# Kernel tuning notes

Hardware: AMD Instinct MI355X
Metric: run time of the kernel (lower is better)

The kernel has to match this reference:

```python
import jax, jax.numpy as jnp
import numpy as np
import math

B = 2        # batch
S = 4095     # input sequence (cls token makes L = 4096)
F_IN = 32    # input feature size
D = 512      # d_model (hidden_size)
H = 8        # n_heads
E = D // H   # head dim = 64
DFF = 2048   # feedforward dim
NL = 2       # encoder layers
FACTOR = 5   # probsparse sampling factor
EPS = 1e-5


def setup_inputs() -> dict:
    key = jax.random.key(0)
    ks = jax.random.split(key, 16)

    def w(k, shape):
        return jax.random.normal(k, shape, dtype=jnp.float32) * 0.02

    inp = {}
    inp['x'] = jax.random.normal(ks[0], (B, S, F_IN), dtype=jnp.float32)
    inp['We'] = w(ks[1], (D, F_IN)); inp['be'] = jnp.zeros((D,), jnp.float32)
    inp['cls'] = jnp.zeros((1, 1, D), jnp.float32)
    inp['Wq'] = w(ks[2], (NL, D, D)); inp['bq'] = jnp.zeros((NL, D), jnp.float32)
    inp['Wk'] = w(ks[3], (NL, D, D)); inp['bk'] = jnp.zeros((NL, D), jnp.float32)
    inp['Wv'] = w(ks[4], (NL, D, D)); inp['bv'] = jnp.zeros((NL, D), jnp.float32)
    inp['Wo'] = w(ks[5], (NL, D, D)); inp['bo'] = jnp.zeros((NL, D), jnp.float32)
    inp['g1'] = jnp.ones((NL, D), jnp.float32); inp['b1'] = jnp.zeros((NL, D), jnp.float32)
    inp['g2'] = jnp.ones((NL, D), jnp.float32); inp['b2'] = jnp.zeros((NL, D), jnp.float32)
    inp['W1'] = w(ks[6], (NL, DFF, D)); inp['bf1'] = jnp.zeros((NL, DFF), jnp.float32)
    inp['W2'] = w(ks[7], (NL, D, DFF)); inp['bf2'] = jnp.zeros((NL, D), jnp.float32)
    inp['Wf'] = w(ks[8], (1, D)); inp['bf'] = jnp.zeros((1,), jnp.float32)
    return inp


def pos_encoding(L):
    # Sinusoidal positional encoding [L, D]
    pos = jnp.arange(L, dtype=jnp.float32)[:, None]
    div = jnp.exp(jnp.arange(0, D, 2, dtype=jnp.float32) * (-math.log(10000.0) / D))
    pe = jnp.zeros((L, D), jnp.float32)
    pe = pe.at[:, 0::2].set(jnp.sin(pos * div))
    pe = pe.at[:, 1::2].set(jnp.cos(pos * div))
    return pe


def layer_norm(x, g, b):
    mu = x.mean(-1, keepdims=True)
    var = ((x - mu) ** 2).mean(-1, keepdims=True)
    return (x - mu) / jnp.sqrt(var + EPS) * g + b


def prob_attention(q, k, v, rng):
    # q, k, v: [B, H, L, E]; mask_flag=False (encoder self-attention)
    b, h, L, e = q.shape
    u = min(FACTOR * int(np.ceil(np.log(L))), L)  # sample_k == n_top here (L_Q == L_K)
    idx = jax.random.randint(rng, (L, u), 0, L)   # random K sampling per query position
    Ks = k[:, :, idx, :]                          # [B,H,L,u,E] gather
    QKs = jnp.einsum('bhle,bhlue->bhlu', q, Ks)   # sampled scores
    M = QKs.max(-1) - QKs.sum(-1) / L             # sparsity measure [B,H,L]
    _, top = jax.lax.top_k(M, u)                  # active query indices [B,H,u]
    Qr = jnp.take_along_axis(q, top[..., None], axis=2)      # [B,H,u,E]
    scores = jnp.einsum('bhue,bhke->bhuk', Qr, k) / math.sqrt(e)
    attn = jax.nn.softmax(scores, axis=-1)
    ctx = jnp.broadcast_to(v.mean(axis=2, keepdims=True), (b, h, L, e))  # initial context = mean(V)
    upd = jnp.einsum('bhuk,bhke->bhue', attn, v)
    bi = jnp.arange(b)[:, None, None]
    hi = jnp.arange(h)[None, :, None]
    ctx = ctx.at[bi, hi, top].set(upd)            # scatter active-query contexts
    return ctx                                    # [B,H,L,E]


def attention_layer(x, Wq_, bq_, Wk_, bk_, Wv_, bv_, Wo_, bo_, rng):
    b, L, _ = x.shape
    q = (x @ Wq_.T + bq_).reshape(b, L, H, E).transpose(0, 2, 1, 3)
    k = (x @ Wk_.T + bk_).reshape(b, L, H, E).transpose(0, 2, 1, 3)
    v = (x @ Wv_.T + bv_).reshape(b, L, H, E).transpose(0, 2, 1, 3)
    ctx = prob_attention(q, k, v, rng)            # [B,H,L,E]
    out = ctx.transpose(0, 2, 1, 3).reshape(b, L, D)
    return out @ Wo_.T + bo_


def reference(x, We, be, cls, Wq, bq, Wk, bk, Wv, bv, Wo, bo, g1, b1, g2, b2, W1, bf1, W2, bf2, Wf, bf):
    h = x @ We.T + be                                            # [B,S,D]
    h = jnp.concatenate([jnp.broadcast_to(cls, (B, 1, D)), h], axis=1)  # prepend cls
    L = h.shape[1]
    h = h + pos_encoding(L)[None]
    for l in range(NL):
        rng = jax.random.fold_in(jax.random.key(42), l)
        a = attention_layer(h, Wq[l], bq[l], Wk[l], bk[l], Wv[l], bv[l], Wo[l], bo[l], rng)
        h = layer_norm(h + a, g1[l], b1[l])
        y = jax.nn.relu(h @ W1[l].T + bf1[l])
        y = y @ W2[l].T + bf2[l]
        h = layer_norm(h + y, g2[l], b2[l])
    return h[:, 0] @ Wf.T + bf  # cls-token prediction head [B,1]
```

## Files before the change

### kernel.cpp

```cpp
#include <hip/hip_runtime.h>
#include <hip/hip_bf16.h>
#include <math.h>
#include <stdint.h>

#define B 2
#define S 4095
#define LSEQ 4096
#define F_IN 32
#define D 512
#define H 8
#define E 64
#define DFF 2048
#define NL 2
#define U 45
#define EPSL 1e-5f
#define LU (LSEQ * U)
#define HALF_LU (LU / 2)
#define NS 32
#define SLICE 128
#define CASTBLK 3074

typedef __attribute__((ext_vector_type(8))) short short8;
typedef __attribute__((ext_vector_type(4))) float f32x4;

#define GLD(gp, lp)                                                            \
    __builtin_amdgcn_global_load_lds(                                          \
        (const __attribute__((address_space(1))) void*)(gp),                   \
        (__attribute__((address_space(3))) void*)(lp), 16, 0, 0)

__device__ __forceinline__ unsigned short bf16_bits(float f) {
    __hip_bfloat16 h = __float2bfloat16(f);
    return *(unsigned short*)&h;
}
__device__ __forceinline__ float bits_to_f32(unsigned short s) {
    union { uint32_t u; float f; } c;
    c.u = ((uint32_t)s) << 16;
    return c.f;
}
__device__ __forceinline__ unsigned long long mkey(float v, int index) {
    uint32_t u = __float_as_uint(v);
    uint32_t mono = (u & 0x80000000u) ? ~u : (u | 0x80000000u);
    return ((unsigned long long)mono << 32) | (uint32_t)(0xFFFFFFFFu - (uint32_t)index);
}

#define TF_BODY(k0, k1, c0, c1, o0, o1)                                        \
    do {                                                                       \
        uint32_t ks2 = (k0) ^ (k1) ^ 0x1BD11BDAu;                              \
        uint32_t x0 = (c0) + (k0), x1 = (c1) + (k1);                           \
        x0 += x1; x1 = ((x1 << 13) | (x1 >> 19)); x1 ^= x0;                    \
        x0 += x1; x1 = ((x1 << 15) | (x1 >> 17)); x1 ^= x0;                    \
        x0 += x1; x1 = ((x1 << 26) | (x1 >> 6));  x1 ^= x0;                    \
        x0 += x1; x1 = ((x1 << 6) | (x1 >> 26));  x1 ^= x0;                    \
        x0 += (k1); x1 += ks2 + 1u;                                            \
        x0 += x1; x1 = ((x1 << 17) | (x1 >> 15)); x1 ^= x0;                    \
        x0 += x1; x1 = ((x1 << 29) | (x1 >> 3));  x1 ^= x0;                    \
        x0 += x1; x1 = ((x1 << 16) | (x1 >> 16)); x1 ^= x0;                    \
        x0 += x1; x1 = ((x1 << 24) | (x1 >> 8));  x1 ^= x0;                    \
        x0 += ks2; x1 += (k0) + 2u;                                            \
        x0 += x1; x1 = ((x1 << 13) | (x1 >> 19)); x1 ^= x0;                    \
        x0 += x1; x1 = ((x1 << 15) | (x1 >> 17)); x1 ^= x0;                    \
        x0 += x1; x1 = ((x1 << 26) | (x1 >> 6));  x1 ^= x0;                    \
        x0 += x1; x1 = ((x1 << 6) | (x1 >> 26));  x1 ^= x0;                    \
        x0 += (k0); x1 += (k1) + 3u;                                           \
        x0 += x1; x1 = ((x1 << 17) | (x1 >> 15)); x1 ^= x0;                    \
        x0 += x1; x1 = ((x1 << 29) | (x1 >> 3));  x1 ^= x0;                    \
        x0 += x1; x1 = ((x1 << 16) | (x1 >> 16)); x1 ^= x0;                    \
        x0 += x1; x1 = ((x1 << 24) | (x1 >> 8));  x1 ^= x0;                    \
        x0 += (k1); x1 += ks2 + 4u;                                            \
        x0 += x1; x1 = ((x1 << 13) | (x1 >> 19)); x1 ^= x0;                    \
        x0 += x1; x1 = ((x1 << 15) | (x1 >> 17)); x1 ^= x0;                    \
        x0 += x1; x1 = ((x1 << 26) | (x1 >> 6));  x1 ^= x0;                    \
        x0 += x1; x1 = ((x1 << 6) | (x1 >> 26));  x1 ^= x0;                    \
        x0 += ks2; x1 += (k0) + 5u;                                            \
        (o0) = x0; (o1) = x1;                                                  \
    } while (0)

__device__ __forceinline__ void threefry_dev(uint32_t k0, uint32_t k1, uint32_t c0,
                                             uint32_t c1, uint32_t& o0, uint32_t& o1) {
    TF_BODY(k0, k1, c0, c1, o0, o1);
}
static void threefry_host(uint32_t k0, uint32_t k1, uint32_t c0, uint32_t c1,
                          uint32_t& o0, uint32_t& o1) {
    TF_BODY(k0, k1, c0, c1, o0, o1);
}

__global__ void prep_cast_kernel(const float* __restrict__ x, const float* __restrict__ We,
                                 __hip_bfloat16* __restrict__ xbf,
                                 __hip_bfloat16* __restrict__ webf,
                                 const float* __restrict__ Wq,
                                 const float* __restrict__ Wk,
                                 const float* __restrict__ Wv,
                                 const float* __restrict__ Wo,
                                 const float* __restrict__ W1,
                                 const float* __restrict__ W2,
                                 const float* __restrict__ bq,
                                 const float* __restrict__ bk,
                                 const float* __restrict__ bv,
                                 __hip_bfloat16* __restrict__ wpool,
                                 float* __restrict__ qkvbias) {
    const int SDD = D * D / 4;
    const int SFD = DFF * D / 4;
    const int CAST_N = 4 * SDD + 2 * SFD;
    const size_t WPL = (size_t)4 * D * D + 2 * (size_t)DFF * D;
    int bid = blockIdx.x;
    int tid = threadIdx.x;
    if (bid < 2 * CASTBLK) {
        int l = bid / CASTBLK;
        int u = (bid % CASTBLK) * 256 + tid;
        __hip_bfloat16* base = wpool + (size_t)l * WPL;
        if (u >= CAST_N) {
            int j = u - CAST_N;
            if (j < 384) {
                int seg = (j * 4) >> 9;
                int off = (j * 4) & 511;
                const float* src = (seg == 0) ? bq + l * D
                                 : (seg == 1) ? bk + l * D : bv + l * D;
                *(float4*)(qkvbias + l * 1536 + j * 4) = *(const float4*)(src + off);
            }
            return;
        }
        const float* src;
        __hip_bfloat16* dst;
        int off;
        if (u < SDD)            { src = Wq + (size_t)l * D * D;   dst = base;                       off = u; }
        else if (u < 2 * SDD)   { src = Wk + (size_t)l * D * D;   dst = base + (size_t)D * D;       off = u - SDD; }
        else if (u < 3 * SDD)   { src = Wv + (size_t)l * D * D;   dst = base + (size_t)2 * D * D;   off = u - 2 * SDD; }
        else if (u < 4 * SDD)   { src = Wo + (size_t)l * D * D;   dst = base + (size_t)3 * D * D;   off = u - 3 * SDD; }
        else if (u < 4 * SDD + SFD) { src = W1 + (size_t)l * DFF * D; dst = base + (size_t)4 * D * D; off = u - 4 * SDD; }
        else { src = W2 + (size_t)l * D * DFF; dst = base + (size_t)4 * D * D + (size_t)DFF * D; off = u - 4 * SDD - SFD; }
        float4 v = ((const float4*)src)[off];
        union { unsigned short s[4]; uint2 w; } o;
        o.s[0] = bf16_bits(v.x); o.s[1] = bf16_bits(v.y);
        o.s[2] = bf16_bits(v.z); o.s[3] = bf16_bits(v.w);
        ((uint2*)dst)[off] = o.w;
    } else {
        int u = (bid - 2 * CASTBLK) * 256 + tid;
        const int NX = B * LSEQ * F_IN / 4;
        const int NW = D * F_IN / 4;
        if (u < NX) {
            int e0 = u * 4;
            int i = e0 & 31;
            int l = (e0 >> 5) & (LSEQ - 1);
            int b = e0 >> 17;
            union { unsigned short s[4]; uint2 w; } o;
            if (l == 0) {
                o.s[0] = o.s[1] = o.s[2] = o.s[3] = 0;
            } else {
                float4 v = *(const float4*)(x + ((size_t)b * S + (l - 1)) * F_IN + i);
                o.s[0] = bf16_bits(v.x); o.s[1] = bf16_bits(v.y);
                o.s[2] = bf16_bits(v.z); o.s[3] = bf16_bits(v.w);
            }
            ((uint2*)xbf)[u] = o.w;
        } else if (u < NX + NW) {
            int w = u - NX;
            float4 v = ((const float4*)We)[w];
            union { unsigned short s[4]; uint2 w2; } o;
            o.s[0] = bf16_bits(v.x); o.s[1] = bf16_bits(v.y);
            o.s[2] = bf16_bits(v.z); o.s[3] = bf16_bits(v.w);
            ((uint2*)webf)[w] = o.w2;
        }
    }
}

__global__ __launch_bounds__(256) void gemm32(const unsigned short* __restrict__ A,
                                              const unsigned short* __restrict__ W,
                                              const float* __restrict__ bias,
                                              float* __restrict__ Cf,
                                              int M, int N, int K) {
    __shared__ unsigned short lds[2 * 128 * 32];
    unsigned short* As = lds;
    unsigned short* Bs = lds + 128 * 32;
    const int tid = threadIdx.x;
    const int m0 = blockIdx.y * 128, n0 = blockIdx.x * 128;
    const int wave = tid >> 6, lane = tid & 63;
    const int wm = (wave >> 1) * 64, wn = (wave & 1) * 64;
    const int quad = lane >> 4, m15 = lane & 15;
    const int srow = tid >> 2, scol = (tid & 3) * 8;
    f32x4 acc[4][4] = {};
    const unsigned short* Ag0 = A + (size_t)(m0 + srow) * K + scol;
    const unsigned short* Ag1 = A + (size_t)(m0 + srow + 64) * K + scol;
    const unsigned short* Wg0 = W + (size_t)(n0 + srow) * K + scol;
    const unsigned short* Wg1 = W + (size_t)(n0 + srow + 64) * K + scol;
    for (int k0 = 0; k0 < K; k0 += 32) {
        __syncthreads();
        GLD(Ag0 + k0, As + tid * 8);
        GLD(Ag1 + k0, As + 2048 + tid * 8);
        GLD(Wg0 + k0, Bs + tid * 8);
        GLD(Wg1 + k0, Bs + 2048 + tid * 8);
        __syncthreads();
        short8 af[4], bfr[4];
#pragma unroll
        for (int mi = 0; mi < 4; ++mi)
            af[mi] = *(const short8*)(As + (wm + mi * 16 + m15) * 32 + quad * 8);
#pragma unroll
        for (int ni = 0; ni < 4; ++ni)
            bfr[ni] = *(const short8*)(Bs + (wn + ni * 16 + m15) * 32 + quad * 8);
#pragma unroll
        for (int mi = 0; mi < 4; ++mi)
#pragma unroll
            for (int ni = 0; ni < 4; ++ni)
                acc[mi][ni] = __builtin_amdgcn_mfma_f32_16x16x32_bf16(
                    af[mi], bfr[ni], acc[mi][ni], 0, 0, 0);
    }
#pragma unroll
    for (int mi = 0; mi < 4; ++mi) {
        int mg = m0 + wm + mi * 16 + quad * 4;
#pragma unroll
        for (int ni = 0; ni < 4; ++ni) {
            int ng = n0 + wn + ni * 16 + m15;
            float bv = bias[ng];
#pragma unroll
            for (int r = 0; r < 4; ++r)
                Cf[(size_t)(mg + r) * N + ng] = acc[mi][ni][r] + bv;
        }
    }
}

__global__ void posenc_kernel(const float* __restrict__ emb, const float* __restrict__ cls,
                              __hip_bfloat16* __restrict__ hbf) {
    int gid = blockIdx.x * blockDim.x + threadIdx.x;
    if (gid >= B * LSEQ * D) return;
    int d = gid % D;
    int l = (gid / D) % LSEQ;
    float v = (l == 0) ? cls[d] : emb[gid];
    int i = d >> 1;
    float divv = expf((float)(2 * i) * (float)(-9.210340371976184 / 512.0));
    float ang = (float)l * divv;
    v += (d & 1) ? cosf(ang) : sinf(ang);
    hbf[gid] = __float2bfloat16(v);
}

template <int MODE>
__global__ __launch_bounds__(256) void gemm_pipe(const unsigned short* __restrict__ A,
                                                 const unsigned short* __restrict__ W,
                                                 const float* __restrict__ bias,
                                                 void* __restrict__ C0,
                                                 void* __restrict__ C1,
                                                 void* __restrict__ C2,
                                                 int M, int N, int K, int NBN) {
    __shared__ unsigned short As[3][128 * 32];
    __shared__ unsigned short Bs[3][128 * 32];
    const int tid = threadIdx.x;
    const int NBM = M >> 7;
    const int bid = blockIdx.x;
    const int xcd = bid & 7, local = bid >> 3;
    const int m_t = xcd * (NBM >> 3) + local / NBN;
    const int n_t = local % NBN;
    const int m0 = m_t * 128, n0 = n_t * 128;
    const int wave = tid >> 6, lane = tid & 63;
    const int wm = (wave >> 1) * 64, wn = (wave & 1) * 64;
    const int quad = lane >> 4, m15 = lane & 15;
    const int srow = tid >> 2, scol = (tid & 3) * 8;
    f32x4 acc[4][4] = {};
    const unsigned short* Ag0 = A + (size_t)(m0 + srow) * K + scol;
    const unsigned short* Ag1 = A + (size_t)(m0 + srow + 64) * K + scol;
    const unsigned short* Wg0 = W + (size_t)(n0 + srow) * K + scol;
    const unsigned short* Wg1 = W + (size_t)(n0 + srow + 64) * K + scol;
#define STAGE_P(buf, k0)                                                       \
    do {                                                                       \
        GLD(Ag0 + (k0), As[buf] + tid * 8);                                    \
        GLD(Ag1 + (k0), As[buf] + 2048 + tid * 8);                             \
        GLD(Wg0 + (k0), Bs[buf] + tid * 8);                                    \
        GLD(Wg1 + (k0), Bs[buf] + 2048 + tid * 8);                             \
    } while (0)
    const int NIT = K >> 5;
    STAGE_P(0, 0);
    STAGE_P(1, 32);
    for (int i = 0; i < NIT; ++i) {
        int cur = i % 3;
        if (i + 2 < NIT) STAGE_P((i + 2) % 3, (i + 2) * 32);
        int rem = NIT - 1 - i;
        if (rem >= 2)      asm volatile("s_waitcnt vmcnt(8)" ::: "memory");
        else if (rem == 1) asm volatile("s_waitcnt vmcnt(4)" ::: "memory");
        else               asm volatile("s_waitcnt vmcnt(0)" ::: "memory");
        __builtin_amdgcn_sched_barrier(0);
        __builtin_amdgcn_s_barrier();
        __builtin_amdgcn_sched_barrier(0);
        short8 af[4], bfr[4];
#pragma unroll
        for (int mi = 0; mi < 4; ++mi)
            af[mi] = *(const short8*)(As[cur] + (wm + mi * 16 + m15) * 32 + quad * 8);
#pragma unroll
        for (int ni = 0; ni < 4; ++ni)
            bfr[ni] = *(const short8*)(Bs[cur] + (wn + ni * 16 + m15) * 32 + quad * 8);
        asm volatile("s_waitcnt lgkmcnt(0)" ::: "memory");
        __builtin_amdgcn_sched_barrier(0);
        __builtin_amdgcn_s_barrier();
        __builtin_amdgcn_sched_barrier(0);
#pragma unroll
        for (int mi = 0; mi < 4; ++mi)
#pragma unroll
            for (int ni = 0; ni < 4; ++ni)
                acc[mi][ni] = __builtin_amdgcn_mfma_f32_16x16x32_bf16(
                    af[mi], bfr[ni], acc[mi][ni], 0, 0, 0);
    }
#undef STAGE_P
#pragma unroll
    for (int mi = 0; mi < 4; ++mi) {
        int mg = m0 + wm + mi * 16 + quad * 4;
#pragma unroll
        for (int ni = 0; ni < 4; ++ni) {
            int ng = n0 + wn + ni * 16 + m15;
            float bv = bias[ng];
#pragma unroll
            for (int r = 0; r < 4; ++r) {
                float v = acc[mi][ni][r] + bv;
                if (MODE == 1) {
                    ((__hip_bfloat16*)C0)[(size_t)(mg + r) * N + ng] = __float2bfloat16(v);
                } else if (MODE == 2) {
                    ((__hip_bfloat16*)C0)[(size_t)(mg + r) * N + ng] =
                        __float2bfloat16(fmaxf(v, 0.f));
                } else {
                    int seg = ng >> 9;
                    int col = ng & 511;
                    __hip_bfloat16* dst = (seg == 0) ? (__hip_bfloat16*)C0
                                        : (seg == 1) ? (__hip_bfloat16*)C1
                                                     : (__hip_bfloat16*)C2;
                    dst[(size_t)(mg + r) * D + col] = __float2bfloat16(v);
                }
            }
        }
    }
}

__global__ __launch_bounds__(256) void gemm_w2b(const unsigned short* __restrict__ A,
                                                const unsigned short* __restrict__ W,
                                                const float* __restrict__ bias,
                                                float* __restrict__ C0,
                                                float* __restrict__ C1) {
    const int K = 2048, N = 512, KH = 1024;
    __shared__ unsigned short As[2][128 * 32];
    __shared__ unsigned short Bs[2][128 * 32];
    const int tid = threadIdx.x;
    const int bid = blockIdx.x;
    const int xcd = bid & 7, local = bid >> 3;
    const int m_t = xcd * 8 + (local >> 3);
    const int n_t = (local >> 1) & 3;
    const int ks = local & 1;
    const int m0 = m_t * 128, n0 = n_t * 128, kb = ks * KH;
    const int wave = tid >> 6, lane = tid & 63;
    const int wm = (wave >> 1) * 64, wn = (wave & 1) * 64;
    const int quad = lane >> 4, m15 = lane & 15;
    const int srow = tid >> 2, scol = (tid & 3) * 8;
    f32x4 acc[4][4] = {};
    const unsigned short* Ag0 = A + (size_t)(m0 + srow) * K + kb + scol;
    const unsigned short* Ag1 = A + (size_t)(m0 + srow + 64) * K + kb + scol;
    const unsigned short* Wg0 = W + (size_t)(n0 + srow) * K + kb + scol;
    const unsigned short* Wg1 = W + (size_t)(n0 + srow + 64) * K + kb + scol;
    GLD(Ag0, As[0] + tid * 8);
    GLD(Ag1, As[0] + 2048 + tid * 8);
    GLD(Wg0, Bs[0] + tid * 8);
    GLD(Wg1, Bs[0] + 2048 + tid * 8);
    int cur = 0;
    for (int k0 = 0; k0 < KH; k0 += 32) {
        __syncthreads();
        int kn = k0 + 32;
        if (kn < KH) {
            GLD(Ag0 + kn, As[cur ^ 1] + tid * 8);
            GLD(Ag1 + kn, As[cur ^ 1] + 2048 + tid * 8);
            GLD(Wg0 + kn, Bs[cur ^ 1] + tid * 8);
            GLD(Wg1 + kn, Bs[cur ^ 1] + 2048 + tid * 8);
        }
        short8 af[4], bfr[4];
#pragma unroll
        for (int mi = 0; mi < 4; ++mi)
            af[mi] = *(const short8*)(As[cur] + (wm + mi * 16 + m15) * 32 + quad * 8);
#pragma unroll
        for (int ni = 0; ni < 4; ++ni)
            bfr[ni] = *(const short8*)(Bs[cur] + (wn + ni * 16 + m15) * 32 + quad * 8);
#pragma unroll
        for (int mi = 0; mi < 4; ++mi)
#pragma unroll
            for (int ni = 0; ni < 4; ++ni)
                acc[mi][ni] = __builtin_amdgcn_mfma_f32_16x16x32_bf16(
                    af[mi], bfr[ni], acc[mi][ni], 0, 0, 0);
        cur ^= 1;
    }
    float* Cf = ks ? C1 : C0;
#pragma unroll
    for (int mi = 0; mi < 4; ++mi) {
        int mg = m0 + wm + mi * 16 + quad * 4;
#pragma unroll
        for (int ni = 0; ni < 4; ++ni) {
            int ng = n0 + wn + ni * 16 + m15;
            float bv = ks ? 0.f : bias[ng];
#pragma unroll
            for (int r = 0; r < 4; ++r)
                Cf[(size_t)(mg + r) * N + ng] = acc[mi][ni][r] + bv;
        }
    }
}

__global__ __launch_bounds__(256) void mscore_kernel(const __hip_bfloat16* __restrict__ qbf,
                                                     const __hip_bfloat16* __restrict__ kbf,
                                                     uint32_t k2a, uint32_t k2b,
                                                     float* __restrict__ Mv,
                                                     float* __restrict__ acorr) {
    __shared__ float Sbuf[U][8];
    __shared__ int sidx[U];
    int bid = blockIdx.x;
    int tid = threadIdx.x;
    if (bid >= B * LSEQ) {
        int vb = bid - B * LSEQ;
        float4 z = {0.f, 0.f, 0.f, 0.f};
        float4* p = (float4*)acorr;
#pragma unroll
        for (int i = 0; i < 32; ++i)
            p[(size_t)i * 32768 + vb * 256 + tid] = z;
        return;
    }
    int b = bid & 1;
    int l = bid >> 1;
    int wave = tid >> 6, lane = tid & 63;
    if (tid < U) {
        int i = l * U + tid;
        uint32_t c0 = (i < HALF_LU) ? (uint32_t)i : (uint32_t)(i - HALF_LU);
        uint32_t o0, o1;
        threefry_dev(k2a, k2b, c0, c0 + HALF_LU, o0, o1);
        sidx[tid] = (int)(((i < HALF_LU) ? o0 : o1) & 4095u);
    }
    const unsigned short* qr =
        (const unsigned short*)qbf + ((size_t)(b * LSEQ) + l) * D + lane * 8;
    union { uint4 u; unsigned short s[8]; } qv;
    qv.u = *(const uint4*)qr;
    float qa[8];
#pragma unroll
    for (int j = 0; j < 8; ++j) qa[j] = bits_to_f32(qv.s[j]);
    __syncthreads();
    const unsigned short* kbase = (const unsigned short*)(kbf + (size_t)(b * LSEQ) * D);
    for (int t = wave; t < U; t += 12) {
        int tb = t + 4, tc = t + 8;
        bool hb = tb < U, hc = tc < U;
        union { uint4 u; unsigned short s[8]; } kva, kvb, kvc;
        kva.u = *(const uint4*)(kbase + (size_t)sidx[t] * D + lane * 8);
        if (hb) kvb.u = *(const uint4*)(kbase + (size_t)sidx[tb] * D + lane * 8);
        if (hc) kvc.u = *(const uint4*)(kbase + (size_t)sidx[tc] * D + lane * 8);
        {
            float p = 0.f;
#pragma unroll
            for (int j = 0; j < 8; ++j) p += qa[j] * bits_to_f32(kva.s[j]);
            p += __shfl_xor(p, 1);
            p += __shfl_xor(p, 2);
            p += __shfl_xor(p, 4);
            if ((lane & 7) == 0) Sbuf[t][lane >> 3] = p;
        }
        if (hb) {
            float p = 0.f;
#pragma unroll
            for (int j = 0; j < 8; ++j) p += qa[j] * bits_to_f32(kvb.s[j]);
            p += __shfl_xor(p, 1);
            p += __shfl_xor(p, 2);
            p += __shfl_xor(p, 4);
            if ((lane & 7) == 0) Sbuf[tb][lane >> 3] = p;
        }
        if (hc) {
            float p = 0.f;
#pragma unroll
            for (int j = 0; j < 8; ++j) p += qa[j] * bits_to_f32(kvc.s[j]);
            p += __shfl_xor(p, 1);
            p += __shfl_xor(p, 2);
            p += __shfl_xor(p, 4);
            if ((lane & 7) == 0) Sbuf[tc][lane >> 3] = p;
        }
    }
    __syncthreads();
    if (tid < 8) {
        float mx = -INFINITY, sm = 0.f;
        for (int t = 0; t < U; ++t) {
            float v = Sbuf[t][tid];
            mx = fmaxf(mx, v);
            sm += v;
        }
        Mv[((size_t)b * H + tid) * LSEQ + l] = mx - sm / (float)LSEQ;
    }
}

__global__ __launch_bounds__(256) void topk_chunk_kernel(const float* __restrict__ Mv,
                                                         unsigned long long* __restrict__ cand) {
    __shared__ unsigned long long sk[256];
    int blk = blockIdx.x;
    int chunk = blk & 15, bh = blk >> 4;
    int tid = threadIdx.x;
    int gi = chunk * 256 + tid;
    sk[tid] = mkey(Mv[(size_t)bh * LSEQ + gi], gi);
    __syncthreads();
    for (int k = 2; k <= 256; k <<= 1) {
        for (int j = k >> 1; j > 0; j >>= 1) {
            int ixj = tid ^ j;
            if (ixj > tid) {
                unsigned long long a = sk[tid], b = sk[ixj];
                bool desc = ((tid & k) == 0);
                if (desc ? (a < b) : (a > b)) { sk[tid] = b; sk[ixj] = a; }
            }
            __syncthreads();
        }
    }
    if (tid < U) cand[((size_t)bh * 16 + chunk) * U + tid] = sk[tid];
}

__global__ __launch_bounds__(256) void topkmerge_vmean_kernel(
        const unsigned long long* __restrict__ cand, int* __restrict__ top,
        const __hip_bfloat16* __restrict__ v, float* __restrict__ part,
        unsigned char* __restrict__ flags) {
    __shared__ unsigned long long sk[1024];
    __shared__ float red[4][64];
    int blk = blockIdx.x;
    int tid = threadIdx.x;
    if (blk < B * H) {
        int bh = blk;
        for (int e = tid; e < 1024; e += 256)
            sk[e] = (e < 16 * U) ? cand[(size_t)bh * 16 * U + e] : 0ull;
        __syncthreads();
        for (int k = 2; k <= 1024; k <<= 1) {
            for (int j = k >> 1; j > 0; j >>= 1) {
                for (int e = tid; e < 1024; e += 256) {
                    int ixj = e ^ j;
                    if (ixj > e) {
                        unsigned long long a = sk[e], b = sk[ixj];
                        bool desc = ((e & k) == 0);
                        if (desc ? (a < b) : (a > b)) { sk[e] = b; sk[ixj] = a; }
                    }
                }
                __syncthreads();
            }
        }
        if (tid < U)
            top[bh * U + tid] = (int)(0xFFFFFFFFu - (uint32_t)(sk[tid] & 0xFFFFFFFFu));
    } else if (blk < B * H + B * H * 8) {
        int vb = blk - B * H;
        int seg = vb & 7, hh = (vb >> 3) & 7, b = vb >> 6;
        int e = tid & 63, rg = tid >> 6;
        const __hip_bfloat16* vp =
            v + ((size_t)(b * LSEQ) + seg * 512) * D + hh * 64 + e;
        float acc = 0.f;
        for (int r = rg; r < 512; r += 4) acc += __bfloat162float(vp[(size_t)r * D]);
        red[rg][e] = acc;
        __syncthreads();
        if (tid < 64)
            part[(size_t)vb * 64 + tid] =
                red[0][tid] + red[1][tid] + red[2][tid] + red[3][tid];
    } else {
        int fb = blk - (B * H + B * H * 8);
        ((int*)flags)[fb * 256 + tid] = 0;
    }
}

__global__ __launch_bounds__(256) void attnred_wobase_kernel(
        const float* __restrict__ Opart, const float* __restrict__ msum,
        const float* __restrict__ vpart, const unsigned short* __restrict__ wob,
        const int* __restrict__ top, float* __restrict__ acorr,
        unsigned char* __restrict__ flags, const float* __restrict__ bo,
        float* __restrict__ base) {
    __shared__ float dlt[E];
    int bid = blockIdx.x;
    int tid = threadIdx.x;
    if (bid < B * H * U) {
        int t = bid % U;
        int bh = bid / U;
        int b = bh >> 3, hh = bh & 7;
        if (tid < 64) {
            int lane = tid;
            float m_s = -INFINITY, ss = 0.f;
            if (lane < NS) {
                size_t base2 = (((size_t)bh * NS + lane) * U + t) * 2;
                m_s = msum[base2];
                ss = msum[base2 + 1];
            }
            float M = m_s;
            for (int off = 32; off; off >>= 1) M = fmaxf(M, __shfl_xor(M, off));
            float e_s = (lane < NS) ? __expf(m_s - M) : 0.f;
            float d = ss * e_s;
            for (int off = 32; off; off >>= 1) d += __shfl_xor(d, off);
            float acc = 0.f;
            for (int s = 0; s < NS; ++s) {
                float w = __shfl(e_s, s);
                acc += w * Opart[(((size_t)bh * NS + s) * U + t) * 64 + lane];
            }
            float vmv = 0.f;
#pragma unroll
            for (int s = 0; s < 8; ++s) vmv += vpart[((size_t)bh * 8 + s) * 64 + lane];
            dlt[lane] = acc / d - vmv / (float)LSEQ;
        }
        __syncthreads();
        int r = top[bh * U + t];
        if (tid == 0) flags[b * LSEQ + r] = 1;
        float* arow = acorr + (size_t)(b * LSEQ + r) * D;
        for (int n = tid; n < D; n += 256) {
            const unsigned short* wr = wob + (size_t)n * D + hh * E;
            float acc = 0.f;
#pragma unroll
            for (int v4 = 0; v4 < 8; ++v4) {
                union { uint4 u; unsigned short s[8]; } w;
                w.u = *(const uint4*)(wr + v4 * 8);
#pragma unroll
                for (int j = 0; j < 8; ++j)
                    acc += dlt[v4 * 8 + j] * bits_to_f32(w.s[j]);
            }
            atomicAdd(arow + n, acc);
        }
    } else {
        int wb = bid - B * H * U;
        int b = wb >> 7;
        int n = (wb & 127) * 4 + (tid >> 6);
        int lane = tid & 63;
        float vmv[8];
#pragma unroll
        for (int j = 0; j < 8; ++j) {
            int idx = lane * 8 + j;
            int hh = idx >> 6, e = idx & 63;
            float acc = 0.f;
#pragma unroll
            for (int s = 0; s < 8; ++s)
                acc += vpart[((size_t)(b * 8 + hh) * 8 + s) * 64 + e];
            vmv[j] = acc / (float)LSEQ;
        }
        union { uint4 u; unsigned short s[8]; } w;
        w.u = *(const uint4*)(wob + (size_t)n * D + lane * 8);
        float p = vmv[0] * bits_to_f32(w.s[0]) + vmv[1] * bits_to_f32(w.s[1]) +
                  vmv[2] * bits_to_f32(w.s[2]) + vmv[3] * bits_to_f32(w.s[3]) +
                  vmv[4] * bits_to_f32(w.s[4]) + vmv[5] * bits_to_f32(w.s[5]) +
                  vmv[6] * bits_to_f32(w.s[6]) + vmv[7] * bits_to_f32(w.s[7]);
        for (int off = 32; off; off >>= 1) p += __shfl_xor(p, off);
        if (lane == 0) base[(size_t)b * D + n] = p + bo[n];
    }
}

__global__ __launch_bounds__(256) void attn_part(const __hip_bfloat16* __restrict__ qbf,
                                                 const __hip_bfloat16* __restrict__ kbf,
                                                 const __hip_bfloat16* __restrict__ vbf,
                                                 const int* __restrict__ top,
                                                 float* __restrict__ Opart,
                                                 float* __restrict__ msum) {
    __shared__ unsigned short Qs[48 * 72];
    __shared__ unsigned short Ks[SLICE * 72];
    __shared__ unsigned short Vs[SLICE * 68];
    __shared__ unsigned short Ps[48 * 136];
    __shared__ float mred[48][4];
    __shared__ float sred[48][4];
    const int slice = blockIdx.x, hh = blockIdx.y, b = blockIdx.z;
    const int bh = b * H + hh;
    const int tid = threadIdx.x;
    const int s0 = slice * SLICE;
    for (int i = tid; i < 48 * 64; i += 256) {
        int t = i >> 6, e = i & 63;
        unsigned short v = 0;
        if (t < U) {
            int r = top[bh * U + t];
            v = ((const unsigned short*)qbf)[((size_t)(b * LSEQ) + r) * D + hh * E + e];
        }
        Qs[t * 72 + e] = v;
    }
    {
        const uint4* src = (const uint4*)(kbf + ((size_t)(b * LSEQ) + s0) * D + hh * E);
        for (int i = tid; i < SLICE * 8; i += 256) {
            int r = i >> 3, c = i & 7;
            uint4 d = src[(size_t)r * 64 + c];
            *(uint4*)(Ks + r * 72 + c * 8) = d;
        }
    }
    {
        const uint2* src = (const uint2*)(vbf + ((size_t)(b * LSEQ) + s0) * D + hh * E);
        for (int i = tid; i < SLICE * 16; i += 256) {
            int r = i >> 4, c = i & 15;
            uint2 d = src[(size_t)r * 128 + c];
            *(uint2*)(Vs + r * 68 + c * 4) = d;
        }
    }
    __syncthreads();
    const int wave = tid >> 6, lane = tid & 63;
    const int quad = lane >> 4, m15 = lane & 15;
    const int wc = wave * 32;
    f32x4 acc[3][2] = {};
#pragma unroll
    for (int ks = 0; ks < 2; ++ks) {
        short8 af[3], bfr[2];
#pragma unroll
        for (int mt = 0; mt < 3; ++mt)
            af[mt] = *(const short8*)(Qs + (mt * 16 + m15) * 72 + ks * 32 + quad * 8);
#pragma unroll
        for (int nt = 0; nt < 2; ++nt)
            bfr[nt] = *(const short8*)(Ks + (wc + nt * 16 + m15) * 72 + ks * 32 + quad * 8);
#pragma unroll
        for (int mt = 0; mt < 3; ++mt)
#pragma unroll
            for (int nt = 0; nt < 2; ++nt)
                acc[mt][nt] = __builtin_amdgcn_mfma_f32_16x16x32_bf16(
                    af[mt], bfr[nt], acc[mt][nt], 0, 0, 0);
    }
    float sc[3][2][4];
#pragma unroll
    for (int mt = 0; mt < 3; ++mt)
#pragma unroll
        for (int nt = 0; nt < 2; ++nt)
#pragma unroll
            for (int r = 0; r < 4; ++r) sc[mt][nt][r] = acc[mt][nt][r] * 0.125f;
#pragma unroll
    for (int mt = 0; mt < 3; ++mt)
#pragma unroll
        for (int r = 0; r < 4; ++r) {
            float mv = fmaxf(sc[mt][0][r], sc[mt][1][r]);
            mv = fmaxf(mv, __shfl_xor(mv, 1));
            mv = fmaxf(mv, __shfl_xor(mv, 2));
            mv = fmaxf(mv, __shfl_xor(mv, 4));
            mv = fmaxf(mv, __shfl_xor(mv, 8));
            if (m15 == 0) mred[mt * 16 + quad * 4 + r][wave] = mv;
        }
    __syncthreads();
#pragma unroll
    for (int mt = 0; mt < 3; ++mt)
#pragma unroll
        for (int r = 0; r < 4; ++r) {
            int row = mt * 16 + quad * 4 + r;
            float ms = fmaxf(fmaxf(mred[row][0], mred[row][1]),
                             fmaxf(mred[row][2], mred[row][3]));
            float p0 = __expf(sc[mt][0][r] - ms);
            float p1 = __expf(sc[mt][1][r] - ms);
            float sv = p0 + p1;
            sv += __shfl_xor(sv, 1);
            sv += __shfl_xor(sv, 2);
            sv += __shfl_xor(sv, 4);
            sv += __shfl_xor(sv, 8);
            if (m15 == 0) sred[row][wave] = sv;
            Ps[row * 136 + wc + m15] = bf16_bits(p0);
            Ps[row * 136 + wc + 16 + m15] = bf16_bits(p1);
        }
    __syncthreads();
    if (tid < U) {
        float mm = fmaxf(fmaxf(mred[tid][0], mred[tid][1]),
                         fmaxf(mred[tid][2], mred[tid][3]));
        float ss = sred[tid][0] + sred[tid][1] + sred[tid][2] + sred[tid][3];
        size_t base = (((size_t)bh * NS + slice) * U + tid) * 2;
        msum[base] = mm;
        msum[base + 1] = ss;
    }
    f32x4 apv[3] = {};
#pragma unroll
    for (int ks = 0; ks < 4; ++ks) {
        short8 bv;
#pragma unroll
        for (int j = 0; j < 8; ++j)
            bv[j] = (short)Vs[(ks * 32 + quad * 8 + j) * 68 + wave * 16 + m15];
        short8 af2[3];
#pragma unroll
        for (int mt = 0; mt < 3; ++mt)
            af2[mt] = *(const short8*)(Ps + (mt * 16 + m15) * 136 + ks * 32 + quad * 8);
#pragma unroll
        for (int mt = 0; mt < 3; ++mt)
            apv[mt] = __builtin_amdgcn_mfma_f32_16x16x32_bf16(af2[mt], bv, apv[mt], 0, 0, 0);
    }
    size_t obase = ((size_t)bh * NS + slice) * U;
#pragma unroll
    for (int mt = 0; mt < 3; ++mt)
#pragma unroll
        for (int r = 0; r < 4; ++r) {
            int row = mt * 16 + quad * 4 + r;
            if (row < U)
                Opart[(obase + row) * 64 + wave * 16 + m15] = apv[mt][r];
        }
}

__global__ __launch_bounds__(64) void add_ln_base_kernel(__hip_bfloat16* __restrict__ hbf,
                                                         const float* __restrict__ base,
                                                         const float* __restrict__ acorr,
                                                         const unsigned char* __restrict__ flags,
                                                         const float* __restrict__ g,
                                                         const float* __restrict__ bb) {
    int row = blockIdx.x;
    int b = row >> 12;
    int lane = threadIdx.x;
    unsigned short* hp = (unsigned short*)hbf + (size_t)row * D;
    const float* bp = base + (size_t)b * D;
    const float* ap = acorr + (size_t)row * D;
    bool has = flags[row] != 0;
    float x[8];
    float sum = 0.f;
#pragma unroll
    for (int j = 0; j < 8; ++j) {
        float a = bp[lane + 64 * j];
        if (has) a += ap[lane + 64 * j];
        x[j] = bits_to_f32(hp[lane + 64 * j]) + a;
        sum += x[j];
    }
    for (int off = 32; off; off >>= 1) sum += __shfl_xor(sum, off);
    float mu = sum / (float)D;
    float vs = 0.f;
#pragma unroll
    for (int j = 0; j < 8; ++j) {
        float dd = x[j] - mu;
        vs += dd * dd;
    }
    for (int off = 32; off; off >>= 1) vs += __shfl_xor(vs, off);
    float inv = 1.f / sqrtf(vs / (float)D + EPSL);
#pragma unroll
    for (int j = 0; j < 8; ++j) {
        float o = (x[j] - mu) * inv * g[lane + 64 * j] + bb[lane + 64 * j];
        hp[lane + 64 * j] = bf16_bits(o);
    }
}

__global__ __launch_bounds__(64) void add_ln_kernel(__hip_bfloat16* __restrict__ hbf,
                                                    const float* __restrict__ a,
                                                    const float* __restrict__ a2,
                                                    const float* __restrict__ g,
                                                    const float* __restrict__ bb,
                                                    const float* __restrict__ Wf,
                                                    const float* __restrict__ bf,
                                                    float* __restrict__ out,
                                                    int fuseFinal) {
    int row = blockIdx.x;
    int lane = threadIdx.x;
    unsigned short* hp = (unsigned short*)hbf + (size_t)row * D;
    const float* ap = a + (size_t)row * D;
    const float* ap2 = a2 + (size_t)row * D;
    float x[8];
    float sum = 0.f;
#pragma unroll
    for (int j = 0; j < 8; ++j) {
        x[j] = bits_to_f32(hp[lane + 64 * j]) + ap[lane + 64 * j] + ap2[lane + 64 * j];
        sum += x[j];
    }
    for (int off = 32; off; off >>= 1) sum += __shfl_xor(sum, off);
    float mu = sum / (float)D;
    float vs = 0.f;
#pragma unroll
    for (int j = 0; j < 8; ++j) {
        float dd = x[j] - mu;
        vs += dd * dd;
    }
    for (int off = 32; off; off >>= 1) vs += __shfl_xor(vs, off);
    float inv = 1.f / sqrtf(vs / (float)D + EPSL);
    bool doFinal = fuseFinal && ((row & (LSEQ - 1)) == 0);
    float facc = 0.f;
#pragma unroll
    for (int j = 0; j < 8; ++j) {
        float o = (x[j] - mu) * inv * g[lane + 64 * j] + bb[lane + 64 * j];
        unsigned short ob = bf16_bits(o);
        hp[lane + 64 * j] = ob;
        if (doFinal) facc += bits_to_f32(ob) * Wf[lane + 64 * j];
    }
    if (doFinal) {
        for (int off = 32; off; off >>= 1) facc += __shfl_xor(facc, off);
        if (lane == 0) out[row >> 12] = facc + bf[0];
    }
}

extern "C" void kernel_launch(void* const* d_in, const int* in_sizes, int n_in,
                              void* d_out, int out_size, void* d_ws, size_t ws_size,
                              hipStream_t stream) {
    (void)in_sizes; (void)n_in; (void)out_size; (void)ws_size;
    const float* x   = (const float*)d_in[0];
    const float* We  = (const float*)d_in[1];
    const float* be  = (const float*)d_in[2];
    const float* cls = (const float*)d_in[3];
    const float* Wq  = (const float*)d_in[4];
    const float* bq  = (const float*)d_in[5];
    const float* Wk  = (const float*)d_in[6];
    const float* bk  = (const float*)d_in[7];
    const float* Wv  = (const float*)d_in[8];
    const float* bv  = (const float*)d_in[9];
    const float* Wo  = (const float*)d_in[10];
    const float* bo  = (const float*)d_in[11];
    const float* g1  = (const float*)d_in[12];
    const float* b1  = (const float*)d_in[13];
    const float* g2  = (const float*)d_in[14];
    const float* b2  = (const float*)d_in[15];
    const float* W1  = (const float*)d_in[16];
    const float* bf1 = (const float*)d_in[17];
    const float* W2  = (const float*)d_in[18];
    const float* bf2 = (const float*)d_in[19];
    const float* Wf  = (const float*)d_in[20];
    const float* bff = (const float*)d_in[21];
    float* out = (float*)d_out;

    float* ws = (float*)d_ws;
    const size_t NT = (size_t)B * LSEQ * D;
    float* aout = ws + NT;
    __hip_bfloat16* kbf    = (__hip_bfloat16*)(ws + NT);
    __hip_bfloat16* q_bf   = (__hip_bfloat16*)(ws + 2 * NT);
    __hip_bfloat16* y1_bf  = (__hip_bfloat16*)(ws + 2 * NT);
    __hip_bfloat16* v_bf   = (__hip_bfloat16*)(ws + 4 * NT);
    __hip_bfloat16* h_bf   = (__hip_bfloat16*)(ws + 5 * NT);
    float* emb   = ws;
    float* acorr = ws;
    float* tmp   = ws;
    float* Opart = ws + 3 * NT;
    float* msumb = Opart + (size_t)B * H * NS * U * 64;
    float* wpool = ws + 5 * NT + NT / 2;
    const size_t WPL = (size_t)4 * D * D + 2 * (size_t)DFF * D;
    __hip_bfloat16* wpool_bf = (__hip_bfloat16*)wpool;
    float* after_w = wpool + (2 * WPL) / 2;
    float* Mbuf = after_w;
    int* top    = (int*)(Mbuf + (size_t)B * H * LSEQ);
    float* vpart  = (float*)(top + B * H * U);
    float* baseb  = vpart + (size_t)128 * 64;
    __hip_bfloat16* xbf  = (__hip_bfloat16*)(baseb + (size_t)B * D);
    __hip_bfloat16* webf = xbf + (size_t)B * LSEQ * F_IN;
    unsigned long long* cand =
        (unsigned long long*)(((uintptr_t)(webf + (size_t)D * F_IN) + 7) & ~(uintptr_t)7);
    float* qkvbias = (float*)(cand + (size_t)B * H * 16 * U);
    unsigned char* flags = (unsigned char*)(qkvbias + 2 * 1536);

    const int ML = B * LSEQ;
    dim3 gD(D / 128, ML / 128);
    const int NPREP = (B * LSEQ * F_IN / 4 + D * F_IN / 4 + 255) / 256;

    prep_cast_kernel<<<2 * CASTBLK + NPREP, 256, 0, stream>>>(
        x, We, xbf, webf, Wq, Wk, Wv, Wo, W1, W2, bq, bk, bv, wpool_bf, qkvbias);
    gemm32<<<gD, 256, 0, stream>>>((const unsigned short*)xbf,
                                   (const unsigned short*)webf, be, emb, ML, D, F_IN);
    posenc_kernel<<<(B * LSEQ * D + 255) / 256, 256, 0, stream>>>(emb, cls, h_bf);

    for (int l = 0; l < NL; ++l) {
        uint32_t f0, f1, a0, a1, bb0, bb1;
        threefry_host(0u, 42u, 0u, (uint32_t)l, f0, f1);
        threefry_host(f0, f1, 0u, 2u, a0, a1);
        threefry_host(f0, f1, 1u, 3u, bb0, bb1);
        (void)a0; (void)bb0;

        __hip_bfloat16* wqb = wpool_bf + (size_t)l * WPL;
        __hip_bfloat16* wob = wqb + (size_t)3 * D * D;
        __hip_bfloat16* w1b = wqb + (size_t)4 * D * D;
        __hip_bfloat16* w2b = w1b + (size_t)DFF * D;

        gemm_pipe<3><<<768, 256, 0, stream>>>((const unsigned short*)h_bf,
                                              (const unsigned short*)wqb,
                                              qkvbias + (size_t)l * 1536,
                                              q_bf, kbf, v_bf, ML, 3 * D, D, 12);

        mscore_kernel<<<B * LSEQ + 128, 256, 0, stream>>>(q_bf, kbf, a1, bb1, Mbuf,
                                                          acorr);
        topk_chunk_kernel<<<B * H * 16, 256, 0, stream>>>(Mbuf, cand);
        topkmerge_vmean_kernel<<<B * H + B * H * 8 + 8, 256, 0, stream>>>(
            cand, top, v_bf, vpart, flags);
        attn_part<<<dim3(NS, H, B), 256, 0, stream>>>(q_bf, kbf, v_bf, top, Opart, msumb);
        attnred_wobase_kernel<<<B * H * U + B * 128, 256, 0, stream>>>(
            Opart, msumb, vpart, (const unsigned short*)wob, top, acorr, flags,
            bo + l * D, baseb);
        add_ln_base_kernel<<<ML, 64, 0, stream>>>(h_bf, baseb, acorr, flags,
                                                  g1 + l * D, b1 + l * D);

        gemm_pipe<2><<<1024, 256, 0, stream>>>((const unsigned short*)h_bf,
                                               (const unsigned short*)w1b, bf1 + l * DFF,
                                               y1_bf, nullptr, nullptr, ML, DFF, D, 16);
        gemm_w2b<<<512, 256, 0, stream>>>((const unsigned short*)y1_bf,
                                          (const unsigned short*)w2b, bf2 + l * D,
                                          aout, tmp);
        add_ln_kernel<<<ML, 64, 0, stream>>>(h_bf, aout, tmp, g2 + l * D, b2 + l * D,
                                             Wf, bff, out, (l == NL - 1) ? 1 : 0);
    }
}
```

Before: 542.9 us.

## Triple-buffer W2 GEMM loads and process two query rows per mscore block

The W2 GEMM moves from double to triple-buffered LDS staging, with explicit vmcnt waits and barriers so that two tiles of global loads stay in flight while MFMAs run on the current tile. Separately, the sampled-score kernel now handles two query rows per block, halving its block count and giving each wave more independent key loads. The GEMM change uses more LDS, which may cut occupancy, and adds a second barrier per iteration. The mscore change raises per-block work and register use.

```diff
diff --git a/kernel.cpp b/kernel.cpp
--- a/kernel.cpp
+++ b/kernel.cpp
@@ -329,8 +329,8 @@
                                                 float* __restrict__ C0,
                                                 float* __restrict__ C1) {
     const int K = 2048, N = 512, KH = 1024;
-    __shared__ unsigned short As[2][128 * 32];
-    __shared__ unsigned short Bs[2][128 * 32];
+    __shared__ unsigned short As[3][128 * 32];
+    __shared__ unsigned short Bs[3][128 * 32];
     const int tid = threadIdx.x;
     const int bid = blockIdx.x;
     const int xcd = bid & 7, local = bid >> 3;
@@ -347,20 +347,26 @@
     const unsigned short* Ag1 = A + (size_t)(m0 + srow + 64) * K + kb + scol;
     const unsigned short* Wg0 = W + (size_t)(n0 + srow) * K + kb + scol;
     const unsigned short* Wg1 = W + (size_t)(n0 + srow + 64) * K + kb + scol;
-    GLD(Ag0, As[0] + tid * 8);
-    GLD(Ag1, As[0] + 2048 + tid * 8);
-    GLD(Wg0, Bs[0] + tid * 8);
-    GLD(Wg1, Bs[0] + 2048 + tid * 8);
-    int cur = 0;
-    for (int k0 = 0; k0 < KH; k0 += 32) {
-        __syncthreads();
-        int kn = k0 + 32;
-        if (kn < KH) {
-            GLD(Ag0 + kn, As[cur ^ 1] + tid * 8);
-            GLD(Ag1 + kn, As[cur ^ 1] + 2048 + tid * 8);
-            GLD(Wg0 + kn, Bs[cur ^ 1] + tid * 8);
-            GLD(Wg1 + kn, Bs[cur ^ 1] + 2048 + tid * 8);
-        }
+#define STAGE_W(buf, k0)                                                       \
+    do {                                                                       \
+        GLD(Ag0 + (k0), As[buf] + tid * 8);                                    \
+        GLD(Ag1 + (k0), As[buf] + 2048 + tid * 8);                             \
+        GLD(Wg0 + (k0), Bs[buf] + tid * 8);                                    \
+        GLD(Wg1 + (k0), Bs[buf] + 2048 + tid * 8);                             \
+    } while (0)
+    const int NIT = KH >> 5;
+    STAGE_W(0, 0);
+    STAGE_W(1, 32);
+    for (int i = 0; i < NIT; ++i) {
+        int cur = i % 3;
+        if (i + 2 < NIT) STAGE_W((i + 2) % 3, (i + 2) * 32);
+        int rem = NIT - 1 - i;
+        if (rem >= 2)      asm volatile("s_waitcnt vmcnt(8)" ::: "memory");
+        else if (rem == 1) asm volatile("s_waitcnt vmcnt(4)" ::: "memory");
+        else               asm volatile("s_waitcnt vmcnt(0)" ::: "memory");
+        __builtin_amdgcn_sched_barrier(0);
+        __builtin_amdgcn_s_barrier();
+        __builtin_amdgcn_sched_barrier(0);
         short8 af[4], bfr[4];
 #pragma unroll
         for (int mi = 0; mi < 4; ++mi)
@@ -368,14 +374,18 @@
 #pragma unroll
         for (int ni = 0; ni < 4; ++ni)
             bfr[ni] = *(const short8*)(Bs[cur] + (wn + ni * 16 + m15) * 32 + quad * 8);
+        asm volatile("s_waitcnt lgkmcnt(0)" ::: "memory");
+        __builtin_amdgcn_sched_barrier(0);
+        __builtin_amdgcn_s_barrier();
+        __builtin_amdgcn_sched_barrier(0);
 #pragma unroll
         for (int mi = 0; mi < 4; ++mi)
 #pragma unroll
             for (int ni = 0; ni < 4; ++ni)
                 acc[mi][ni] = __builtin_amdgcn_mfma_f32_16x16x32_bf16(
                     af[mi], bfr[ni], acc[mi][ni], 0, 0, 0);
-        cur ^= 1;
-    }
+    }
+#undef STAGE_W
     float* Cf = ks ? C1 : C0;
 #pragma unroll
     for (int mi = 0; mi < 4; ++mi) {
@@ -396,12 +406,12 @@
                                                      uint32_t k2a, uint32_t k2b,
                                                      float* __restrict__ Mv,
                                                      float* __restrict__ acorr) {
-    __shared__ float Sbuf[U][8];
-    __shared__ int sidx[U];
+    __shared__ float Sbuf[2][U][8];
+    __shared__ int sidx[2 * U];
     int bid = blockIdx.x;
     int tid = threadIdx.x;
-    if (bid >= B * LSEQ) {
-        int vb = bid - B * LSEQ;
+    if (bid >= B * LSEQ / 2) {
+        int vb = bid - B * LSEQ / 2;
         float4 z = {0.f, 0.f, 0.f, 0.f};
         float4* p = (float4*)acorr;
 #pragma unroll
@@ -410,68 +420,76 @@
         return;
     }
     int b = bid & 1;
-    int l = bid >> 1;
+    int l0 = (bid >> 1) * 2;
     int wave = tid >> 6, lane = tid & 63;
-    if (tid < U) {
-        int i = l * U + tid;
+    if (tid < 2 * U) {
+        int rr = tid / U, uu = tid % U;
+        int i = (l0 + rr) * U + uu;
         uint32_t c0 = (i < HALF_LU) ? (uint32_t)i : (uint32_t)(i - HALF_LU);
         uint32_t o0, o1;
         threefry_dev(k2a, k2b, c0, c0 + HALF_LU, o0, o1);
         sidx[tid] = (int)(((i < HALF_LU) ? o0 : o1) & 4095u);
     }
-    const unsigned short* qr =
-        (const unsigned short*)qbf + ((size_t)(b * LSEQ) + l) * D + lane * 8;
-    union { uint4 u; unsigned short s[8]; } qv;
-    qv.u = *(const uint4*)qr;
-    float qa[8];
-#pragma unroll
-    for (int j = 0; j < 8; ++j) qa[j] = bits_to_f32(qv.s[j]);
+    float qa[2][8];
+#pragma unroll
+    for (int rr = 0; rr < 2; ++rr) {
+        const unsigned short* qr =
+            (const unsigned short*)qbf + ((size_t)(b * LSEQ) + l0 + rr) * D + lane * 8;
+        union { uint4 u; unsigned short s[8]; } qv;
+        qv.u = *(const uint4*)qr;
+#pragma unroll
+        for (int j = 0; j < 8; ++j) qa[rr][j] = bits_to_f32(qv.s[j]);
+    }
     __syncthreads();
     const unsigned short* kbase = (const unsigned short*)(kbf + (size_t)(b * LSEQ) * D);
-    for (int t = wave; t < U; t += 12) {
+    for (int t = wave; t < 2 * U; t += 12) {
         int tb = t + 4, tc = t + 8;
-        bool hb = tb < U, hc = tc < U;
+        bool hb = tb < 2 * U, hc = tc < 2 * U;
         union { uint4 u; unsigned short s[8]; } kva, kvb, kvc;
         kva.u = *(const uint4*)(kbase + (size_t)sidx[t] * D + lane * 8);
         if (hb) kvb.u = *(const uint4*)(kbase + (size_t)sidx[tb] * D + lane * 8);
         if (hc) kvc.u = *(const uint4*)(kbase + (size_t)sidx[tc] * D + lane * 8);
         {
+            const float* q = qa[t / U];
             float p = 0.f;
 #pragma unroll
-            for (int j = 0; j < 8; ++j) p += qa[j] * bits_to_f32(kva.s[j]);
+            for (int j = 0; j < 8; ++j) p += q[j] * bits_to_f32(kva.s[j]);
             p += __shfl_xor(p, 1);
             p += __shfl_xor(p, 2);
             p += __shfl_xor(p, 4);
-            if ((lane & 7) == 0) Sbuf[t][lane >> 3] = p;
+            if ((lane & 7) == 0) Sbuf[t / U][t % U][lane >> 3] = p;
         }
         if (hb) {
+            const float* q = qa[tb / U];
             float p = 0.f;
 #pragma unroll
-            for (int j = 0; j < 8; ++j) p += qa[j] * bits_to_f32(kvb.s[j]);
+            for (int j = 0; j < 8; ++j) p += q[j] * bits_to_f32(kvb.s[j]);
             p += __shfl_xor(p, 1);
             p += __shfl_xor(p, 2);
             p += __shfl_xor(p, 4);
-            if ((lane & 7) == 0) Sbuf[tb][lane >> 3] = p;
+            if ((lane & 7) == 0) Sbuf[tb / U][tb % U][lane >> 3] = p;
         }
         if (hc) {
+            const float* q = qa[tc / U];
             float p = 0.f;
 #pragma unroll
-            for (int j = 0; j < 8; ++j) p += qa[j] * bits_to_f32(kvc.s[j]);
+            for (int j = 0; j < 8; ++j) p += q[j] * bits_to_f32(kvc.s[j]);
             p += __shfl_xor(p, 1);
             p += __shfl_xor(p, 2);
             p += __shfl_xor(p, 4);
-            if ((lane & 7) == 0) Sbuf[tc][lane >> 3] = p;
+            if ((lane & 7) == 0) Sbuf[tc / U][tc % U][lane >> 3] = p;
         }
     }
     __syncthreads();
-    if (tid < 8) {
+    if (tid < 16) {
+        int rr = tid >> 3, hh = tid & 7;
         float mx = -INFINITY, sm = 0.f;
         for (int t = 0; t < U; ++t) {
-            float v = Sbuf[t][tid];
+            float v = Sbuf[rr][t][hh];
             mx = fmaxf(mx, v);
             sm += v;
         }
-        Mv[((size_t)b * H + tid) * LSEQ + l] = mx - sm / (float)LSEQ;
+        Mv[((size_t)b * H + hh) * LSEQ + (l0 + rr)] = mx - sm / (float)LSEQ;
     }
 }
 
@@ -927,8 +945,8 @@
                                               qkvbias + (size_t)l * 1536,
                                               q_bf, kbf, v_bf, ML, 3 * D, D, 12);
 
-        mscore_kernel<<<B * LSEQ + 128, 256, 0, stream>>>(q_bf, kbf, a1, bb1, Mbuf,
-                                                          acorr);
+        mscore_kernel<<<B * LSEQ / 2 + 128, 256, 0, stream>>>(q_bf, kbf, a1, bb1, Mbuf,
+                                                              acorr);
         topk_chunk_kernel<<<B * H * 16, 256, 0, stream>>>(Mbuf, cand);
         topkmerge_vmean_kernel<<<B * H + B * H * 8 + 8, 256, 0, stream>>>(
             cand, top, v_bf, vpart, flags);
```

New measurement: 542.9 us. Within noise of the previous version (+0.0%).
